# Optimization experiments

Hardware: AMD Instinct MI355X
Metric: run time of the kernel (lower is better)

Reference implementation:

```python
import jax, jax.numpy as jnp
import numpy as np

HEAD_SIZE = 128

def setup_inputs() -> dict:
    key = jax.random.key(0)
    ks = jax.random.split(key, 4)
    B, T, C, H = 8, 2048, 1024, HEAD_SIZE
    x = jax.random.normal(ks[0], (B, T, C), dtype=jnp.float32)
    Wk = jax.random.normal(ks[1], (C, H), dtype=jnp.float32) * (C ** -0.5)
    Wq = jax.random.normal(ks[2], (C, H), dtype=jnp.float32) * (C ** -0.5)
    Wv = jax.random.normal(ks[3], (C, H), dtype=jnp.float32) * (C ** -0.5)
    return {"x": x, "Wk": Wk, "Wq": Wq, "Wv": Wv}

def reference(x, Wk, Wq, Wv):
    # x: [B,T,C]; projections to [B,T,H]
    k = jnp.einsum('btc,ch->bth', x, Wk)
    q = jnp.einsum('btc,ch->bth', x, Wq)
    v = jnp.einsum('btc,ch->bth', x, Wv)
    scale = HEAD_SIZE ** -0.5
    wei = jnp.einsum('bqh,bkh->bqk', q, k) * scale  # [B,T,T]
    T = x.shape[1]
    causal = jnp.tril(jnp.ones((T, T), dtype=bool))
    wei = jnp.where(causal, wei, -jnp.inf)
    wei = jax.nn.softmax(wei, axis=-1)
    # dropout p=0 (eval) -> identity
    out = jnp.einsum('bqk,bkh->bqh', wei, v)  # [B,T,H]
    return out
```

## Files before the change

### kernel.cpp

```cpp
#include <hip/hip_runtime.h>

#define B_DIM 8
#define T_DIM 2048
#define C_DIM 1024
#define H_DIM 128

typedef __attribute__((ext_vector_type(8))) short bf16x8;
typedef __attribute__((ext_vector_type(4))) float f32x4;

__device__ __forceinline__ short f2bf(float f) {
  union { float f; unsigned u; } v; v.f = f;
  unsigned u = v.u;
  unsigned r = (u + 0x7FFFu + ((u >> 16) & 1u)) >> 16;
  return (short)r;
}

__device__ __forceinline__ void gload_lds16(const short* g, short* l) {
  __builtin_amdgcn_global_load_lds(
      (const __attribute__((address_space(1))) void*)g,
      (__attribute__((address_space(3))) void*)l, 16, 0, 0);
}

__device__ __forceinline__ float rowmax16(float x) {
  union { float f; int i; } a, t;
  a.f = x;
  t.i = __builtin_amdgcn_update_dpp(a.i, a.i, 0x128, 0xf, 0xf, false);
  a.f = fmaxf(a.f, t.f);
  t.i = __builtin_amdgcn_update_dpp(a.i, a.i, 0x124, 0xf, 0xf, false);
  a.f = fmaxf(a.f, t.f);
  t.i = __builtin_amdgcn_update_dpp(a.i, a.i, 0x122, 0xf, 0xf, false);
  a.f = fmaxf(a.f, t.f);
  t.i = __builtin_amdgcn_update_dpp(a.i, a.i, 0x121, 0xf, 0xf, false);
  a.f = fmaxf(a.f, t.f);
  return a.f;
}
__device__ __forceinline__ float rowsum16(float x) {
  union { float f; int i; } a, t;
  a.f = x;
  t.i = __builtin_amdgcn_update_dpp(a.i, a.i, 0x128, 0xf, 0xf, false);
  a.f += t.f;
  t.i = __builtin_amdgcn_update_dpp(a.i, a.i, 0x124, 0xf, 0xf, false);
  a.f += t.f;
  t.i = __builtin_amdgcn_update_dpp(a.i, a.i, 0x122, 0xf, 0xf, false);
  a.f += t.f;
  t.i = __builtin_amdgcn_update_dpp(a.i, a.i, 0x121, 0xf, 0xf, false);
  a.f += t.f;
  return a.f;
}

#define NXE ((B_DIM * T_DIM * C_DIM) / 8)
#define NWE ((3 * C_DIM * H_DIM) / 8)

__global__ __launch_bounds__(256) void prep_kernel(
    const float* __restrict__ x, const float* __restrict__ Wk,
    const float* __restrict__ Wq, const float* __restrict__ Wv,
    short* __restrict__ xb, short* __restrict__ Wt) {
  int gid = blockIdx.x * 256 + threadIdx.x;
  if (gid < NXE) {
    const float* src = x + (size_t)gid * 8;
    float4 f0 = ((const float4*)src)[0];
    float4 f1 = ((const float4*)src)[1];
    __attribute__((aligned(16))) short t[8];
    t[0] = f2bf(f0.x); t[1] = f2bf(f0.y); t[2] = f2bf(f0.z); t[3] = f2bf(f0.w);
    t[4] = f2bf(f1.x); t[5] = f2bf(f1.y); t[6] = f2bf(f1.z); t[7] = f2bf(f1.w);
    ((int4*)xb)[gid] = *(const int4*)t;
  } else {
    int j = gid - NXE;
    if (j >= NWE) return;
    int w = j >> 14;
    int r = j & 16383;
    int h = r >> 7;
    int c0 = (r & 127) * 8;
    const float* W = (w == 0) ? Wk : ((w == 1) ? Wq : Wv);
    __attribute__((aligned(16))) short t[8];
#pragma unroll
    for (int i = 0; i < 8; i++) t[i] = f2bf(W[(size_t)(c0 + i) * H_DIM + h]);
    *(int4*)(Wt + (size_t)w * (C_DIM * H_DIM) + h * C_DIM + c0) = *(const int4*)t;
  }
}

__global__ __launch_bounds__(256) void proj_kernel(
    const short* __restrict__ xb, const short* __restrict__ Wt,
    short* __restrict__ Kp, short* __restrict__ Qb, short* __restrict__ Vp) {
  const int wi = blockIdx.y;
  const int m0 = blockIdx.x * 128;
  __shared__ short As[128 * 32];
  __shared__ short Bs[128 * 32];
  const int tid  = threadIdx.x;
  const int lane = tid & 63;
  const int wv   = tid >> 6;
  const int n    = lane & 15;
  const int quad = lane >> 4;
  const int mbase = (wv >> 1) * 64;
  const int nbase = (wv & 1) * 64;
  const short* Wp = Wt + (size_t)wi * (C_DIM * H_DIM);

  const int lr = lane >> 2;
  const int lc = (lane & 3) * 8;

  f32x4 acc[4][4];
#pragma unroll
  for (int i = 0; i < 4; i++)
#pragma unroll
    for (int j = 0; j < 4; j++) {
      f32x4 z = {0.f, 0.f, 0.f, 0.f};
      acc[i][j] = z;
    }

  for (int k0 = 0; k0 < C_DIM; k0 += 32) {
    __syncthreads();
#pragma unroll
    for (int h = 0; h < 2; h++) {
      int ch = wv * 2 + h;
      int row = ch * 16 + lr;
      gload_lds16(xb + (size_t)(m0 + row) * C_DIM + k0 + lc, &As[ch * 512]);
      gload_lds16(Wp + (size_t)row * C_DIM + k0 + lc, &Bs[ch * 512]);
    }
    __syncthreads();

    bf16x8 aF[4], bF[4];
#pragma unroll
    for (int mt = 0; mt < 4; mt++)
      aF[mt] = *(const bf16x8*)&As[(mbase + mt * 16 + n) * 32 + quad * 8];
#pragma unroll
    for (int nt = 0; nt < 4; nt++)
      bF[nt] = *(const bf16x8*)&Bs[(nbase + nt * 16 + n) * 32 + quad * 8];
#pragma unroll
    for (int mt = 0; mt < 4; mt++)
#pragma unroll
      for (int nt = 0; nt < 4; nt++)
        acc[mt][nt] = __builtin_amdgcn_mfma_f32_16x16x32_bf16(
            aF[mt], bF[nt], acc[mt][nt], 0, 0, 0);
  }

#pragma unroll
  for (int mt = 0; mt < 4; mt++) {
#pragma unroll
    for (int nt = 0; nt < 4; nt++) {
#pragma unroll
      for (int i = 0; i < 4; i++) {
        int row = m0 + mbase + mt * 16 + quad * 4 + i;
        int col = nbase + nt * 16 + n;
        short v = f2bf(acc[mt][nt][i]);
        int bb = row >> 11;
        int t  = row & (T_DIM - 1);
        int tt = t >> 6;
        if (wi == 0) {
          int rr = t & 63;
          int knt = rr >> 4, kn = rr & 15;
          int kc = col >> 5, kq = (col >> 3) & 3, kj = col & 7;
          Kp[(((size_t)(bb * 32 + tt) * 16 + knt * 4 + kc) * 512) +
             (kq * 16 + kn) * 8 + kj] = v;
        } else if (wi == 1) {
          Qb[(size_t)row * H_DIM + col] = v;
        } else {
          int vkc = (t >> 5) & 1, vq = (t >> 3) & 3, vj = t & 7;
          int ht = col >> 4, vn = col & 15;
          Vp[(((size_t)(bb * 32 + tt) * 16 + ht * 2 + vkc) * 512) +
             (vq * 16 + vn) * 8 + vj] = v;
        }
      }
    }
  }
}

__global__ __launch_bounds__(256, 4) void attn_kernel(
    const short* __restrict__ Qb, const short* __restrict__ Kp,
    const short* __restrict__ Vp, float* __restrict__ out) {
  const int id = blockIdx.y * 128 + blockIdx.x;
  const int b  = id & 7;
  const int qt = id >> 3;
  const int q0 = qt * 16;
  const int tid  = threadIdx.x;
  const int lane = tid & 63;
  const int g    = tid >> 6;
  const int n    = lane & 15;
  const int quad = lane >> 4;

  __shared__ short Ps[4][16][72];
  __shared__ float Om[16][128];
  __shared__ float Ml[16][2];

  const int ntiles = (qt >> 2) + 1;
  const float scale = 0.08838834764831845f;
  const int row0 = q0 + quad * 4;

  const short* Kbase = Kp + (size_t)b * 32 * 16 * 512;
  const short* Vbase = Vp + (size_t)b * 32 * 16 * 512;

  bf16x8 aQ[4];
  {
    const short* qrow = Qb + (size_t)(b * T_DIM + q0 + n) * H_DIM;
#pragma unroll
    for (int kc = 0; kc < 4; kc++)
      aQ[kc] = *(const bf16x8*)(qrow + kc * 32 + quad * 8);
  }

  f32x4 accO[8];
#pragma unroll
  for (int i = 0; i < 8; i++) {
    f32x4 z = {0.f, 0.f, 0.f, 0.f};
    accO[i] = z;
  }
  float mrow[4] = {-1e30f, -1e30f, -1e30f, -1e30f};
  float lrow[4] = {0.f, 0.f, 0.f, 0.f};

  for (int t = g; t < ntiles; t += 4) {
    const int j0 = t * 64;
    const short* Kt = Kbase + (size_t)t * 16 * 512 + lane * 8;
    const short* Vt = Vbase + (size_t)t * 16 * 512 + lane * 8;
    f32x4 accS[4];
#pragma unroll
    for (int nt = 0; nt < 4; nt++) {
      f32x4 z = {0.f, 0.f, 0.f, 0.f};
      accS[nt] = z;
    }
    bf16x8 fr[8];
#pragma unroll
    for (int nt = 0; nt < 2; nt++)
#pragma unroll
      for (int kc = 0; kc < 4; kc++)
        fr[nt * 4 + kc] = *(const bf16x8*)(Kt + (nt * 4 + kc) * 512);
    __builtin_amdgcn_sched_barrier(0);
#pragma unroll
    for (int nt = 0; nt < 2; nt++)
#pragma unroll
      for (int kc = 0; kc < 4; kc++)
        accS[nt] = __builtin_amdgcn_mfma_f32_16x16x32_bf16(
            aQ[kc], fr[nt * 4 + kc], accS[nt], 0, 0, 0);
    __builtin_amdgcn_sched_barrier(0);
#pragma unroll
    for (int nt = 0; nt < 2; nt++)
#pragma unroll
      for (int kc = 0; kc < 4; kc++)
        fr[nt * 4 + kc] = *(const bf16x8*)(Kt + ((nt + 2) * 4 + kc) * 512);
    __builtin_amdgcn_sched_barrier(0);
#pragma unroll
    for (int nt = 0; nt < 2; nt++)
#pragma unroll
      for (int kc = 0; kc < 4; kc++)
        accS[nt + 2] = __builtin_amdgcn_mfma_f32_16x16x32_bf16(
            aQ[kc], fr[nt * 4 + kc], accS[nt + 2], 0, 0, 0);
    __builtin_amdgcn_sched_barrier(0);

    float mt4[4] = {-1e30f, -1e30f, -1e30f, -1e30f};
#pragma unroll
    for (int nt = 0; nt < 4; nt++) {
      int col = j0 + nt * 16 + n;
#pragma unroll
      for (int i = 0; i < 4; i++) {
        float s = accS[nt][i] * scale;
        s = (col > row0 + i) ? -1e30f : s;
        accS[nt][i] = s;
        mt4[i] = fmaxf(mt4[i], s);
      }
    }
#pragma unroll
    for (int i = 0; i < 4; i++) mt4[i] = rowmax16(mt4[i]);

    bf16x8 frv[8];
#pragma unroll
    for (int ht = 0; ht < 4; ht++)
#pragma unroll
      for (int kc = 0; kc < 2; kc++)
        frv[ht * 2 + kc] = *(const bf16x8*)(Vt + (ht * 2 + kc) * 512);
    __builtin_amdgcn_sched_barrier(0);

    float alpha[4], rsum[4];
#pragma unroll
    for (int i = 0; i < 4; i++) {
      float mnew = fmaxf(mrow[i], mt4[i]);
      alpha[i] = __expf(mrow[i] - mnew);
      mrow[i] = mnew;
      rsum[i] = 0.f;
    }
#pragma unroll
    for (int nt = 0; nt < 4; nt++)
#pragma unroll
      for (int i = 0; i < 4; i++) {
        float p = __expf(accS[nt][i] - mrow[i]);
        rsum[i] += p;
        Ps[g][quad * 4 + i][nt * 16 + n] = f2bf(p);
      }
#pragma unroll
    for (int i = 0; i < 4; i++) {
      rsum[i] = rowsum16(rsum[i]);
      lrow[i] = lrow[i] * alpha[i] + rsum[i];
    }
#pragma unroll
    for (int ht = 0; ht < 8; ht++)
#pragma unroll
      for (int i = 0; i < 4; i++)
        accO[ht][i] *= alpha[i];

    asm volatile("s_waitcnt lgkmcnt(0)" ::: "memory");
    __builtin_amdgcn_sched_barrier(0);

    bf16x8 aP[2];
#pragma unroll
    for (int kc = 0; kc < 2; kc++)
      aP[kc] = *(const bf16x8*)&Ps[g][n][kc * 32 + quad * 8];

#pragma unroll
    for (int ht = 0; ht < 4; ht++)
#pragma unroll
      for (int kc = 0; kc < 2; kc++)
        accO[ht] = __builtin_amdgcn_mfma_f32_16x16x32_bf16(
            aP[kc], frv[ht * 2 + kc], accO[ht], 0, 0, 0);
    __builtin_amdgcn_sched_barrier(0);
#pragma unroll
    for (int ht = 0; ht < 4; ht++)
#pragma unroll
      for (int kc = 0; kc < 2; kc++)
        frv[ht * 2 + kc] = *(const bf16x8*)(Vt + ((ht + 4) * 2 + kc) * 512);
    __builtin_amdgcn_sched_barrier(0);
#pragma unroll
    for (int ht = 0; ht < 4; ht++)
#pragma unroll
      for (int kc = 0; kc < 2; kc++)
        accO[ht + 4] = __builtin_amdgcn_mfma_f32_16x16x32_bf16(
            aP[kc], frv[ht * 2 + kc], accO[ht + 4], 0, 0, 0);
  }

  __syncthreads();
  if (g == 0) {
#pragma unroll
    for (int i = 0; i < 4; i++) {
      int r = quad * 4 + i;
#pragma unroll
      for (int ht = 0; ht < 8; ht++)
        Om[r][ht * 16 + n] = accO[ht][i];
      if (n == 0) { Ml[r][0] = mrow[i]; Ml[r][1] = lrow[i]; }
    }
  }
#pragma unroll
  for (int gg = 1; gg < 4; gg++) {
    __syncthreads();
    if (g == gg) {
#pragma unroll
      for (int i = 0; i < 4; i++) {
        int r = quad * 4 + i;
        float m1 = Ml[r][0], l1 = Ml[r][1];
        float mnew = fmaxf(mrow[i], m1);
        float a0 = __expf(mrow[i] - mnew);
        float a1 = __expf(m1 - mnew);
        float lnew = lrow[i] * a0 + l1 * a1;
        if (gg < 3) {
          if (n == 0) { Ml[r][0] = mnew; Ml[r][1] = lnew; }
#pragma unroll
          for (int ht = 0; ht < 8; ht++)
            Om[r][ht * 16 + n] = accO[ht][i] * a0 + Om[r][ht * 16 + n] * a1;
        } else {
          float linv = 1.0f / lnew;
          size_t base = (size_t)(b * T_DIM + q0 + r) * H_DIM;
#pragma unroll
          for (int ht = 0; ht < 8; ht++)
            out[base + ht * 16 + n] =
                (accO[ht][i] * a0 + Om[r][ht * 16 + n] * a1) * linv;
        }
      }
    }
  }
}

extern "C" void kernel_launch(void* const* d_in, const int* in_sizes, int n_in,
                              void* d_out, int out_size, void* d_ws, size_t ws_size,
                              hipStream_t stream) {
  (void)in_sizes; (void)n_in; (void)out_size; (void)ws_size;
  const float* x  = (const float*)d_in[0];
  const float* Wk = (const float*)d_in[1];
  const float* Wq = (const float*)d_in[2];
  const float* Wv = (const float*)d_in[3];
  float* out = (float*)d_out;

  char* ws = (char*)d_ws;
  short* Wt = (short*)ws;
  short* Kp = (short*)(ws + 786432);
  short* Qb = (short*)(ws + 786432 + 4194304);
  short* Vp = (short*)(ws + 786432 + 8388608);
  short* xb = (short*)(ws + 786432 + 12582912);

  prep_kernel<<<dim3((NXE + NWE) / 256), dim3(256), 0, stream>>>(x, Wk, Wq, Wv, xb, Wt);
  proj_kernel<<<dim3(128, 3), dim3(256), 0, stream>>>(xb, Wt, Kp, Qb, Vp);
  attn_kernel<<<dim3(128, 8), dim3(256), 0, stream>>>(Qb, Kp, Vp, out);
}
```

Baseline: 178.5 us.

## Fuse x bf16 conversion into projection GEMM and widen attention to eight waves

The separate fp32-to-bf16 pass over x is removed. The projection kernel now reads fp32 x directly, converts it while staging into double-buffered LDS, and computes K, Q and V together in one 64x384 tile per block, which avoids writing and re-reading an intermediate bf16 copy of x. The attention kernel goes to 512 threads with eight waves splitting the KV tiles, uses a tree reduction to merge the partial softmax states, and schedules the longest causal query tiles first. The cost is more LDS per block, more register pressure, and fewer blocks for the projection GEMM.

```diff
diff --git a/kernel.cpp b/kernel.cpp
--- a/kernel.cpp
+++ b/kernel.cpp
@@ -13,12 +13,6 @@
   unsigned u = v.u;
   unsigned r = (u + 0x7FFFu + ((u >> 16) & 1u)) >> 16;
   return (short)r;
-}
-
-__device__ __forceinline__ void gload_lds16(const short* g, short* l) {
-  __builtin_amdgcn_global_load_lds(
-      (const __attribute__((address_space(1))) void*)g,
-      (__attribute__((address_space(3))) void*)l, 16, 0, 0);
 }
 
 __device__ __forceinline__ float rowmax16(float x) {
@@ -48,114 +42,122 @@
   return a.f;
 }
 
-#define NXE ((B_DIM * T_DIM * C_DIM) / 8)
 #define NWE ((3 * C_DIM * H_DIM) / 8)
 
-__global__ __launch_bounds__(256) void prep_kernel(
-    const float* __restrict__ x, const float* __restrict__ Wk,
-    const float* __restrict__ Wq, const float* __restrict__ Wv,
-    short* __restrict__ xb, short* __restrict__ Wt) {
-  int gid = blockIdx.x * 256 + threadIdx.x;
-  if (gid < NXE) {
-    const float* src = x + (size_t)gid * 8;
-    float4 f0 = ((const float4*)src)[0];
-    float4 f1 = ((const float4*)src)[1];
-    __attribute__((aligned(16))) short t[8];
-    t[0] = f2bf(f0.x); t[1] = f2bf(f0.y); t[2] = f2bf(f0.z); t[3] = f2bf(f0.w);
-    t[4] = f2bf(f1.x); t[5] = f2bf(f1.y); t[6] = f2bf(f1.z); t[7] = f2bf(f1.w);
-    ((int4*)xb)[gid] = *(const int4*)t;
-  } else {
-    int j = gid - NXE;
-    if (j >= NWE) return;
-    int w = j >> 14;
-    int r = j & 16383;
-    int h = r >> 7;
-    int c0 = (r & 127) * 8;
-    const float* W = (w == 0) ? Wk : ((w == 1) ? Wq : Wv);
-    __attribute__((aligned(16))) short t[8];
-#pragma unroll
-    for (int i = 0; i < 8; i++) t[i] = f2bf(W[(size_t)(c0 + i) * H_DIM + h]);
-    *(int4*)(Wt + (size_t)w * (C_DIM * H_DIM) + h * C_DIM + c0) = *(const int4*)t;
-  }
-}
-
-__global__ __launch_bounds__(256) void proj_kernel(
-    const short* __restrict__ xb, const short* __restrict__ Wt,
+__global__ __launch_bounds__(256) void wprep_kernel(
+    const float* __restrict__ Wk, const float* __restrict__ Wq,
+    const float* __restrict__ Wv, short* __restrict__ Wt) {
+  int j = blockIdx.x * 256 + threadIdx.x;
+  if (j >= NWE) return;
+  int w = j >> 14;
+  int r = j & 16383;
+  int h = r >> 7;
+  int c0 = (r & 127) * 8;
+  const float* W = (w == 0) ? Wk : ((w == 1) ? Wq : Wv);
+  __attribute__((aligned(16))) short t[8];
+#pragma unroll
+  for (int i = 0; i < 8; i++) t[i] = f2bf(W[(size_t)(c0 + i) * H_DIM + h]);
+  *(int4*)(Wt + (size_t)w * (C_DIM * H_DIM) + h * C_DIM + c0) = *(const int4*)t;
+}
+
+__global__ __launch_bounds__(512) void projf_kernel(
+    const float* __restrict__ x, const short* __restrict__ Wt,
     short* __restrict__ Kp, short* __restrict__ Qb, short* __restrict__ Vp) {
-  const int wi = blockIdx.y;
-  const int m0 = blockIdx.x * 128;
-  __shared__ short As[128 * 32];
-  __shared__ short Bs[128 * 32];
+  const int m0 = blockIdx.x * 64;
+  __shared__ short As[2][64][40];
+  __shared__ short Bs[2][384][40];
   const int tid  = threadIdx.x;
   const int lane = tid & 63;
   const int wv   = tid >> 6;
   const int n    = lane & 15;
   const int quad = lane >> 4;
-  const int mbase = (wv >> 1) * 64;
-  const int nbase = (wv & 1) * 64;
-  const short* Wp = Wt + (size_t)wi * (C_DIM * H_DIM);
-
-  const int lr = lane >> 2;
-  const int lc = (lane & 3) * 8;
-
-  f32x4 acc[4][4];
-#pragma unroll
-  for (int i = 0; i < 4; i++)
-#pragma unroll
-    for (int j = 0; j < 4; j++) {
+  const int mh = wv >> 2;
+  const int nq = wv & 3;
+
+  const int ar = tid >> 3, ac = (tid & 7) * 4;
+  const int br = tid >> 2, bc = (tid & 3) * 8;
+
+  f32x4 acc[2][6];
+#pragma unroll
+  for (int i = 0; i < 2; i++)
+#pragma unroll
+    for (int j = 0; j < 6; j++) {
       f32x4 z = {0.f, 0.f, 0.f, 0.f};
       acc[i][j] = z;
     }
 
-  for (int k0 = 0; k0 < C_DIM; k0 += 32) {
-    __syncthreads();
-#pragma unroll
-    for (int h = 0; h < 2; h++) {
-      int ch = wv * 2 + h;
-      int row = ch * 16 + lr;
-      gload_lds16(xb + (size_t)(m0 + row) * C_DIM + k0 + lc, &As[ch * 512]);
-      gload_lds16(Wp + (size_t)row * C_DIM + k0 + lc, &Bs[ch * 512]);
-    }
-    __syncthreads();
-
-    bf16x8 aF[4], bF[4];
-#pragma unroll
-    for (int mt = 0; mt < 4; mt++)
-      aF[mt] = *(const bf16x8*)&As[(mbase + mt * 16 + n) * 32 + quad * 8];
-#pragma unroll
-    for (int nt = 0; nt < 4; nt++)
-      bF[nt] = *(const bf16x8*)&Bs[(nbase + nt * 16 + n) * 32 + quad * 8];
-#pragma unroll
-    for (int mt = 0; mt < 4; mt++)
-#pragma unroll
-      for (int nt = 0; nt < 4; nt++)
+  float4 ax;
+  int4 bx0, bx1, bx2;
+  const float* xrow = x + (size_t)(m0 + ar) * C_DIM + ac;
+
+  auto LOADG = [&](int k0) {
+    ax  = *(const float4*)(xrow + k0);
+    bx0 = *(const int4*)(Wt + (size_t)br * C_DIM + k0 + bc);
+    bx1 = *(const int4*)(Wt + (size_t)(br + 128) * C_DIM + k0 + bc);
+    bx2 = *(const int4*)(Wt + (size_t)(br + 256) * C_DIM + k0 + bc);
+  };
+  auto STORE = [&](int buf) {
+    __attribute__((aligned(8))) short t4[4];
+    t4[0] = f2bf(ax.x); t4[1] = f2bf(ax.y); t4[2] = f2bf(ax.z); t4[3] = f2bf(ax.w);
+    *(int2*)&As[buf][ar][ac] = *(const int2*)t4;
+    *(int4*)&Bs[buf][br][bc] = bx0;
+    *(int4*)&Bs[buf][br + 128][bc] = bx1;
+    *(int4*)&Bs[buf][br + 256][bc] = bx2;
+  };
+  auto COMPUTE = [&](int buf) {
+    bf16x8 aF[2], bF[6];
+#pragma unroll
+    for (int mt = 0; mt < 2; mt++)
+      aF[mt] = *(const bf16x8*)&As[buf][mh * 32 + mt * 16 + n][quad * 8];
+#pragma unroll
+    for (int nt = 0; nt < 6; nt++)
+      bF[nt] = *(const bf16x8*)&Bs[buf][nq * 96 + nt * 16 + n][quad * 8];
+#pragma unroll
+    for (int mt = 0; mt < 2; mt++)
+#pragma unroll
+      for (int nt = 0; nt < 6; nt++)
         acc[mt][nt] = __builtin_amdgcn_mfma_f32_16x16x32_bf16(
             aF[mt], bF[nt], acc[mt][nt], 0, 0, 0);
-  }
-
-#pragma unroll
-  for (int mt = 0; mt < 4; mt++) {
-#pragma unroll
-    for (int nt = 0; nt < 4; nt++) {
+  };
+
+  LOADG(0);
+  STORE(0);
+  __syncthreads();
+  for (int kk = 0; kk < 32; kk++) {
+    if (kk < 31) LOADG((kk + 1) * 32);
+    COMPUTE(kk & 1);
+    __syncthreads();
+    if (kk < 31) {
+      STORE((kk + 1) & 1);
+      __syncthreads();
+    }
+  }
+
+#pragma unroll
+  for (int mt = 0; mt < 2; mt++) {
+#pragma unroll
+    for (int nt = 0; nt < 6; nt++) {
 #pragma unroll
       for (int i = 0; i < 4; i++) {
-        int row = m0 + mbase + mt * 16 + quad * 4 + i;
-        int col = nbase + nt * 16 + n;
+        int row = m0 + mh * 32 + mt * 16 + quad * 4 + i;
+        int col = nq * 96 + nt * 16 + n;
         short v = f2bf(acc[mt][nt][i]);
+        int w = col >> 7;
+        int c = col & 127;
         int bb = row >> 11;
         int t  = row & (T_DIM - 1);
         int tt = t >> 6;
-        if (wi == 0) {
+        if (w == 0) {
           int rr = t & 63;
           int knt = rr >> 4, kn = rr & 15;
-          int kc = col >> 5, kq = (col >> 3) & 3, kj = col & 7;
+          int kc = c >> 5, kq = (c >> 3) & 3, kj = c & 7;
           Kp[(((size_t)(bb * 32 + tt) * 16 + knt * 4 + kc) * 512) +
              (kq * 16 + kn) * 8 + kj] = v;
-        } else if (wi == 1) {
-          Qb[(size_t)row * H_DIM + col] = v;
+        } else if (w == 1) {
+          Qb[(size_t)row * H_DIM + c] = v;
         } else {
           int vkc = (t >> 5) & 1, vq = (t >> 3) & 3, vj = t & 7;
-          int ht = col >> 4, vn = col & 15;
+          int ht = c >> 4, vn = c & 15;
           Vp[(((size_t)(bb * 32 + tt) * 16 + ht * 2 + vkc) * 512) +
              (vq * 16 + vn) * 8 + vj] = v;
         }
@@ -164,12 +166,12 @@
   }
 }
 
-__global__ __launch_bounds__(256, 4) void attn_kernel(
+__global__ __launch_bounds__(512, 6) void attn_kernel(
     const short* __restrict__ Qb, const short* __restrict__ Kp,
     const short* __restrict__ Vp, float* __restrict__ out) {
   const int id = blockIdx.y * 128 + blockIdx.x;
   const int b  = id & 7;
-  const int qt = id >> 3;
+  const int qt = 127 - (id >> 3);
   const int q0 = qt * 16;
   const int tid  = threadIdx.x;
   const int lane = tid & 63;
@@ -177,9 +179,9 @@
   const int n    = lane & 15;
   const int quad = lane >> 4;
 
-  __shared__ short Ps[4][16][72];
-  __shared__ float Om[16][128];
-  __shared__ float Ml[16][2];
+  __shared__ short Ps[8][16][72];
+  __shared__ float Om[4][16][128];
+  __shared__ float Ml[4][16][2];
 
   const int ntiles = (qt >> 2) + 1;
   const float scale = 0.08838834764831845f;
@@ -205,7 +207,7 @@
   float mrow[4] = {-1e30f, -1e30f, -1e30f, -1e30f};
   float lrow[4] = {0.f, 0.f, 0.f, 0.f};
 
-  for (int t = g; t < ntiles; t += 4) {
+  for (int t = g; t < ntiles; t += 8) {
     const int j0 = t * 64;
     const short* Kt = Kbase + (size_t)t * 16 * 512 + lane * 8;
     const short* Vt = Vbase + (size_t)t * 16 * 512 + lane * 8;
@@ -322,43 +324,57 @@
             aP[kc], frv[ht * 2 + kc], accO[ht + 4], 0, 0, 0);
   }
 
-  __syncthreads();
-  if (g == 0) {
+  auto MWRITE = [&](int s) {
 #pragma unroll
     for (int i = 0; i < 4; i++) {
       int r = quad * 4 + i;
 #pragma unroll
       for (int ht = 0; ht < 8; ht++)
-        Om[r][ht * 16 + n] = accO[ht][i];
-      if (n == 0) { Ml[r][0] = mrow[i]; Ml[r][1] = lrow[i]; }
-    }
-  }
-#pragma unroll
-  for (int gg = 1; gg < 4; gg++) {
-    __syncthreads();
-    if (g == gg) {
-#pragma unroll
-      for (int i = 0; i < 4; i++) {
-        int r = quad * 4 + i;
-        float m1 = Ml[r][0], l1 = Ml[r][1];
-        float mnew = fmaxf(mrow[i], m1);
-        float a0 = __expf(mrow[i] - mnew);
-        float a1 = __expf(m1 - mnew);
-        float lnew = lrow[i] * a0 + l1 * a1;
-        if (gg < 3) {
-          if (n == 0) { Ml[r][0] = mnew; Ml[r][1] = lnew; }
-#pragma unroll
-          for (int ht = 0; ht < 8; ht++)
-            Om[r][ht * 16 + n] = accO[ht][i] * a0 + Om[r][ht * 16 + n] * a1;
-        } else {
-          float linv = 1.0f / lnew;
-          size_t base = (size_t)(b * T_DIM + q0 + r) * H_DIM;
-#pragma unroll
-          for (int ht = 0; ht < 8; ht++)
-            out[base + ht * 16 + n] =
-                (accO[ht][i] * a0 + Om[r][ht * 16 + n] * a1) * linv;
-        }
-      }
+        Om[s][r][ht * 16 + n] = accO[ht][i];
+      if (n == 0) { Ml[s][r][0] = mrow[i]; Ml[s][r][1] = lrow[i]; }
+    }
+  };
+  auto MCOMB = [&](int s) {
+#pragma unroll
+    for (int i = 0; i < 4; i++) {
+      int r = quad * 4 + i;
+      float m1 = Ml[s][r][0], l1 = Ml[s][r][1];
+      float mnew = fmaxf(mrow[i], m1);
+      float a0 = __expf(mrow[i] - mnew);
+      float a1 = __expf(m1 - mnew);
+      mrow[i] = mnew;
+      lrow[i] = lrow[i] * a0 + l1 * a1;
+#pragma unroll
+      for (int ht = 0; ht < 8; ht++)
+        accO[ht][i] = accO[ht][i] * a0 + Om[s][r][ht * 16 + n] * a1;
+    }
+  };
+
+  __syncthreads();
+  if (g & 1) MWRITE(g >> 1);
+  __syncthreads();
+  if (!(g & 1)) MCOMB(g >> 1);
+  __syncthreads();
+  if (!(g & 1) && (g & 2)) MWRITE(g >> 2);
+  __syncthreads();
+  if (!(g & 3)) MCOMB(g >> 2);
+  __syncthreads();
+  if (g == 4) MWRITE(0);
+  __syncthreads();
+  if (g == 0) {
+#pragma unroll
+    for (int i = 0; i < 4; i++) {
+      int r = quad * 4 + i;
+      float m1 = Ml[0][r][0], l1 = Ml[0][r][1];
+      float mnew = fmaxf(mrow[i], m1);
+      float a0 = __expf(mrow[i] - mnew);
+      float a1 = __expf(m1 - mnew);
+      float linv = 1.0f / (lrow[i] * a0 + l1 * a1);
+      size_t base = (size_t)(b * T_DIM + q0 + r) * H_DIM;
+#pragma unroll
+      for (int ht = 0; ht < 8; ht++)
+        out[base + ht * 16 + n] =
+            (accO[ht][i] * a0 + Om[0][r][ht * 16 + n] * a1) * linv;
     }
   }
 }
@@ -378,9 +394,8 @@
   short* Kp = (short*)(ws + 786432);
   short* Qb = (short*)(ws + 786432 + 4194304);
   short* Vp = (short*)(ws + 786432 + 8388608);
-  short* xb = (short*)(ws + 786432 + 12582912);
-
-  prep_kernel<<<dim3((NXE + NWE) / 256), dim3(256), 0, stream>>>(x, Wk, Wq, Wv, xb, Wt);
-  proj_kernel<<<dim3(128, 3), dim3(256), 0, stream>>>(xb, Wt, Kp, Qb, Vp);
-  attn_kernel<<<dim3(128, 8), dim3(256), 0, stream>>>(Qb, Kp, Vp, out);
-}
+
+  wprep_kernel<<<dim3(192), dim3(256), 0, stream>>>(Wk, Wq, Wv, Wt);
+  projf_kernel<<<dim3(256), dim3(512), 0, stream>>>(x, Wt, Kp, Qb, Vp);
+  attn_kernel<<<dim3(128, 8), dim3(512), 0, stream>>>(Qb, Kp, Vp, out);
+}
```

New measurement: 288.2 us. +61.5%, slower.
